# Kernel optimization log

Measured on AMD Instinct MI355X. Metric: run time of the kernel, lower is better.

Reference implementation:

```python
import jax, jax.numpy as jnp
import numpy as np

B, IN, H, OUT, E = 8192, 1024, 4096, 1024, 8
HG = H // 2  # gating hidden

def setup_inputs() -> dict:
    key = jax.random.key(0)
    ks = jax.random.split(key, 9)
    s_in = 1.0 / np.sqrt(IN)
    s_h = 1.0 / np.sqrt(H)
    s_hg = 1.0 / np.sqrt(HG)
    return {
        "x": jax.random.normal(ks[0], (B, IN), jnp.float32),
        # gating MLP: Linear(IN,HG) -> ReLU -> Linear(HG,E) -> softmax
        "gw1": jax.random.uniform(ks[1], (IN, HG), jnp.float32, -s_in, s_in),
        "gb1": jax.random.uniform(ks[2], (HG,), jnp.float32, -s_in, s_in),
        "gw2": jax.random.uniform(ks[3], (HG, E), jnp.float32, -s_hg, s_hg),
        "gb2": jax.random.uniform(ks[4], (E,), jnp.float32, -s_hg, s_hg),
        # experts: E x (Linear(IN,H) -> ReLU -> Linear(H,OUT))
        "ew1": jax.random.uniform(ks[5], (E, IN, H), jnp.float32, -s_in, s_in),
        "eb1": jax.random.uniform(ks[6], (E, H), jnp.float32, -s_in, s_in),
        "ew2": jax.random.uniform(ks[7], (E, H, OUT), jnp.float32, -s_h, s_h),
        "eb2": jax.random.uniform(ks[8], (E, OUT), jnp.float32, -s_h, s_h),
    }

def reference(x, gw1, gb1, gw2, gb2, ew1, eb1, ew2, eb2):
    # Gating network (dropout is a no-op in eval)
    gh = jax.nn.relu(x @ gw1 + gb1)                       # [B, HG]
    gates = jax.nn.softmax(gh @ gw2 + gb2, axis=1)        # [B, E]
    # All experts run on the full batch
    h = jax.nn.relu(jnp.einsum('bi,eih->beh', x, ew1) + eb1[None])  # [B, E, H]
    eo = jnp.einsum('beh,eho->beo', h, ew2) + eb2[None]             # [B, E, OUT]
    # Gate-weighted combine: (stacked * gates[...,None]).sum(dim=1)
    combined = jnp.einsum('beo,be->bo', eo, gates)        # [B, OUT]
    return combined
```

## Files before the change

### kernel.cpp

```cpp
#include <hip/hip_runtime.h>


#define DI __device__ __forceinline__

typedef _Float16 f16;
typedef _Float16 f16x8 __attribute__((ext_vector_type(8)));
typedef float f32x4 __attribute__((ext_vector_type(4)));

constexpr int BSZ  = 8192;
constexpr int IND  = 1024;
constexpr int HID  = 4096;
constexpr int OUTD = 1024;
constexpr int NE   = 8;
constexpr int HGD  = 2048;

__global__ __launch_bounds__(256) void conv_f32_f16_kernel(
    const float* __restrict__ in, f16* __restrict__ out)
{
    size_t i = ((size_t)blockIdx.x * 256 + threadIdx.x) * 8;
    const float4* p = (const float4*)(in + i);
    float4 a = p[0], b = p[1];
    f16x8 v = {(f16)a.x, (f16)a.y, (f16)a.z, (f16)a.w,
               (f16)b.x, (f16)b.y, (f16)b.z, (f16)b.w};
    *(f16x8*)(out + i) = v;
}

__global__ __launch_bounds__(256) void transpose_f32_f16_kernel(
    const float* __restrict__ W, f16* __restrict__ Wt, int K, int N)
{
    __shared__ float t[64][65];
    int n0 = blockIdx.x * 64, k0 = blockIdx.y * 64;
    int tx = threadIdx.x & 63, ty = threadIdx.x >> 6;
#pragma unroll
    for (int i = 0; i < 16; i++) {
        int k = i * 4 + ty;
        t[k][tx] = W[(size_t)(k0 + k) * N + n0 + tx];
    }
    __syncthreads();
#pragma unroll
    for (int i = 0; i < 16; i++) {
        int n = i * 4 + ty;
        Wt[(size_t)(n0 + n) * K + k0 + tx] = (f16)t[tx][n];
    }
}

DI void gload_lds16(const void* g, void* l)
{
    typedef const __attribute__((address_space(1))) unsigned int as1_t;
    typedef __attribute__((address_space(3))) unsigned int as3_t;
    __builtin_amdgcn_global_load_lds(
        (as1_t*)(unsigned long long)(__SIZE_TYPE__)g,
        (as3_t*)(unsigned int)(__SIZE_TYPE__)l,
        16, 0, 0);
}


#define PH(BUF, MH, KS, PRE, STAGE, VM)                                        \
  {                                                                            \
    f16x8 av0 = ldA(BUF, 0, MH, KS);                                           \
    f16x8 av1 = ldA(BUF, 1, MH, KS);                                           \
    f16x8 av2 = ldA(BUF, 2, MH, KS);                                           \
    f16x8 av3 = ldA(BUF, 3, MH, KS);                                           \
    if constexpr ((PRE) >= 0) {                                                \
      _Pragma("unroll")                                                        \
      for (int n = 0; n < NF; n++) breg[n][KS] = ldB(BUF, n, KS);              \
    }                                                                          \
    STAGE                                                                      \
    __builtin_amdgcn_sched_barrier(0);                                         \
    __builtin_amdgcn_s_barrier();                                              \
    asm volatile("s_waitcnt lgkmcnt(0)" ::: "memory");                         \
    __builtin_amdgcn_sched_barrier(0);                                         \
    __builtin_amdgcn_s_setprio(1);                                             \
    _Pragma("unroll")                                                          \
    for (int n = 0; n < NF; n++) {                                             \
      acc[(MH)*4+0][n] = __builtin_amdgcn_mfma_f32_16x16x32_f16(av0, breg[n][KS], acc[(MH)*4+0][n], 0, 0, 0); \
      acc[(MH)*4+1][n] = __builtin_amdgcn_mfma_f32_16x16x32_f16(av1, breg[n][KS], acc[(MH)*4+1][n], 0, 0, 0); \
      acc[(MH)*4+2][n] = __builtin_amdgcn_mfma_f32_16x16x32_f16(av2, breg[n][KS], acc[(MH)*4+2][n], 0, 0, 0); \
      acc[(MH)*4+3][n] = __builtin_amdgcn_mfma_f32_16x16x32_f16(av3, breg[n][KS], acc[(MH)*4+3][n], 0, 0, 0); \
    }                                                                          \
    __builtin_amdgcn_s_setprio(0);                                             \
    VM                                                                         \
    __builtin_amdgcn_sched_barrier(0);                                         \
    __builtin_amdgcn_s_barrier();                                              \
    asm volatile("" ::: "memory");                                             \
  }

#define VMSTEP                                                                 \
  { if (i + 1 == NI) { asm volatile("s_waitcnt vmcnt(0)"); }                   \
    else if constexpr (BN == 256) { asm volatile("s_waitcnt vmcnt(4)"); }      \
    else { asm volatile("s_waitcnt vmcnt(2)"); } }

template <int BN, bool RELU, bool GATE, bool OUT_F16, bool ACCUM>
__global__ __launch_bounds__(512, 2) void gemm8p_kernel(
    const f16* __restrict__ A, const f16* __restrict__ Bt,
    const float* __restrict__ bias, const float* __restrict__ gate,
    void* __restrict__ Cptr, int M, int N, int K)
{
    constexpr int BM = 256, BK = 64;
    constexpr int NF  = BN / 64;
    constexpr int NBC = (BN * BK * 2) / 8192;
    __shared__ __align__(16) f16 sA[2][BM * BK];
    __shared__ __align__(16) f16 sB[2][BN * BK];

    const int tid = threadIdx.x, wid = tid >> 6, lane = tid & 63;
    const int wm = wid >> 2, wn = wid & 3;

    const int nwg = gridDim.x;
    const int bid = blockIdx.x;
    const int wg  = (bid & 7) * (nwg >> 3) + (bid >> 3);
    const int gx  = N / BN;
    const size_t bm = (size_t)(wg / gx) * BM;
    const size_t bn = (size_t)(wg % gx) * BN;

    f32x4 acc[8][NF] = {};
    f16x8 breg[NF][2];

    const int srow = (wid << 3) + (lane >> 3);
    const int scol = ((((lane & 7) << 4) ^ (((lane >> 3) & 7) << 4)) >> 1);
    const f16* Ab = A  + (bm + srow) * (size_t)K + scol;
    const f16* Bb = Bt + (bn + srow) * (size_t)K + scol;
    char* sAb = (char*)&sA[0][0] + wid * 1024;
    char* sBb = (char*)&sB[0][0] + wid * 1024;

    auto stA = [&](int b, int q, int t) {
        gload_lds16(Ab + (size_t)q * 64 * K + t * BK,
                    sAb + b * (BM * BK * 2) + q * 8192);
    };
    auto stB = [&](int b, int q, int t) {
        gload_lds16(Bb + (size_t)q * 64 * K + t * BK,
                    sBb + b * (BN * BK * 2) + q * 8192);
    };
    auto ldA = [&](int b, int f, int mh, int ks) -> f16x8 {
        int r  = wm * 128 + mh * 64 + f * 16 + (lane & 15);
        int kb = (((ks * 32) + ((lane >> 4) << 3)) << 1) ^ ((r & 7) << 4);
        return *(const f16x8*)((const char*)&sA[b][0] + r * 128 + kb);
    };
    auto ldB = [&](int b, int n, int ks) -> f16x8 {
        int r  = wn * (BN / 4) + n * 16 + (lane & 15);
        int kb = (((ks * 32) + ((lane >> 4) << 3)) << 1) ^ ((r & 7) << 4);
        return *(const f16x8*)((const char*)&sB[b][0] + r * 128 + kb);
    };

    const int NT = K / BK, NI = NT / 2;

#pragma unroll
    for (int q = 0; q < 4; q++) stA(0, q, 0);
#pragma unroll
    for (int q = 0; q < NBC; q++) stB(0, q, 0);
#pragma unroll
    for (int q = 0; q < NBC; q++) stB(1, q, 1);
    if constexpr (NBC == 4) { asm volatile("s_waitcnt vmcnt(4)"); }
    else                    { asm volatile("s_waitcnt vmcnt(2)"); }
    __builtin_amdgcn_s_barrier();
    asm volatile("" ::: "memory");

    for (int i = 0; i < NI; ++i) {
        const int t = 2 * i;
        const bool pf = (i + 1 < NI);
        PH(0, 0, 0, 0,
           { stA(1,0,t+1); stA(1,1,t+1); stA(1,2,t+1); stA(1,3,t+1); }, {})
        PH(0, 0, 1, 1, {}, {})
        PH(0, 1, 0, -1,
           { if (pf) { stB(0,0,t+2); stB(0,1,t+2); } }, {})
        PH(0, 1, 1, -1,
           { if (pf) { if constexpr (NBC == 4) { stB(0,2,t+2); stB(0,3,t+2); } } },
           VMSTEP)
        PH(1, 0, 0, 0,
           { if (pf) { stA(0,0,t+2); stA(0,1,t+2); stA(0,2,t+2); stA(0,3,t+2); } }, {})
        PH(1, 0, 1, 1, {}, {})
        PH(1, 1, 0, -1,
           { if (pf) { stB(1,0,t+3); stB(1,1,t+3); } }, {})
        PH(1, 1, 1, -1,
           { if (pf) { if constexpr (NBC == 4) { stB(1,2,t+3); stB(1,3,t+3); } } },
           VMSTEP)
    }

    const size_t row0 = bm + (size_t)wm * 128;
    const int col0 = (int)bn + wn * (BN / 4);
    const int c0 = lane & 15, r0 = (lane >> 4) * 4;
#pragma unroll
    for (int fm = 0; fm < 8; fm++) {
#pragma unroll
        for (int r = 0; r < 4; r++) {
            const size_t row = row0 + fm * 16 + r0 + r;
            float g = 1.0f;
            if constexpr (GATE) g = gate[row * NE];
#pragma unroll
            for (int n = 0; n < NF; n++) {
                const size_t col = (size_t)col0 + n * 16 + c0;
                float v = acc[fm][n][r] + bias[col];
                if constexpr (RELU) v = fmaxf(v, 0.0f);
                if constexpr (GATE) v *= g;
                if constexpr (OUT_F16) {
                    ((f16*)Cptr)[row * (size_t)N + col] = (f16)v;
                } else {
                    float* p = (float*)Cptr + row * (size_t)N + col;
                    *p = ACCUM ? (*p + v) : v;
                }
            }
        }
    }
}

__global__ __launch_bounds__(256) void gate_softmax_kernel(
    const f16* __restrict__ gh, const float* __restrict__ gw2,
    const float* __restrict__ gb2, float* __restrict__ gates)
{
    const int row  = blockIdx.x * 4 + (threadIdx.x >> 6);
    const int lane = threadIdx.x & 63;
    const f16* r = gh + (size_t)row * HGD;
    float acc[NE] = {};
    for (int k = lane; k < HGD; k += 64) {
        float h = (float)r[k];
        const float* w = gw2 + (size_t)k * NE;
#pragma unroll
        for (int e = 0; e < NE; e++) acc[e] = fmaf(h, w[e], acc[e]);
    }
#pragma unroll
    for (int off = 32; off > 0; off >>= 1)
#pragma unroll
        for (int e = 0; e < NE; e++) acc[e] += __shfl_down(acc[e], off, 64);
    if (lane == 0) {
        float l[NE], m = -1e30f;
#pragma unroll
        for (int e = 0; e < NE; e++) { l[e] = acc[e] + gb2[e]; m = fmaxf(m, l[e]); }
        float s = 0.f;
#pragma unroll
        for (int e = 0; e < NE; e++) { l[e] = expf(l[e] - m); s += l[e]; }
        float inv = 1.0f / s;
#pragma unroll
        for (int e = 0; e < NE; e++) gates[(size_t)row * NE + e] = l[e] * inv;
    }
}

extern "C" void kernel_launch(void* const* d_in, const int* in_sizes, int n_in,
                              void* d_out, int out_size, void* d_ws, size_t ws_size,
                              hipStream_t stream)
{
    const float* x   = (const float*)d_in[0];
    const float* gw1 = (const float*)d_in[1];
    const float* gb1 = (const float*)d_in[2];
    const float* gw2 = (const float*)d_in[3];
    const float* gb2 = (const float*)d_in[4];
    const float* ew1 = (const float*)d_in[5];
    const float* eb1 = (const float*)d_in[6];
    const float* ew2 = (const float*)d_in[7];
    const float* eb2 = (const float*)d_in[8];
    float* out = (float*)d_out;

    char* ws = (char*)d_ws;
    float* gates = (float*)ws;
    f16* x16  = (f16*)(ws + (256 << 10));
    f16* wbuf = x16 + (size_t)BSZ * IND;
    f16* hbuf = wbuf + (size_t)HID * IND;
    f16* gh   = hbuf;

    conv_f32_f16_kernel<<<(BSZ * IND) / (256 * 8), 256, 0, stream>>>(x, x16);

    transpose_f32_f16_kernel<<<dim3(HGD / 64, IND / 64), 256, 0, stream>>>(gw1, wbuf, IND, HGD);
    gemm8p_kernel<256, true, false, true, false>
        <<<(HGD / 256) * (BSZ / 256), 512, 0, stream>>>(
            x16, wbuf, gb1, nullptr, gh, BSZ, HGD, IND);

    gate_softmax_kernel<<<BSZ / 4, 256, 0, stream>>>(gh, gw2, gb2, gates);

    for (int e = 0; e < NE; e++) {
        transpose_f32_f16_kernel<<<dim3(HID / 64, IND / 64), 256, 0, stream>>>(
            ew1 + (size_t)e * IND * HID, wbuf, IND, HID);
        gemm8p_kernel<256, true, false, true, false>
            <<<(HID / 256) * (BSZ / 256), 512, 0, stream>>>(
                x16, wbuf, eb1 + (size_t)e * HID, nullptr, hbuf, BSZ, HID, IND);

        transpose_f32_f16_kernel<<<dim3(OUTD / 64, HID / 64), 256, 0, stream>>>(
            ew2 + (size_t)e * HID * OUTD, wbuf, HID, OUTD);
        if (e == 0)
            gemm8p_kernel<128, false, true, false, false>
                <<<(OUTD / 128) * (BSZ / 256), 512, 0, stream>>>(
                    hbuf, wbuf, eb2 + (size_t)e * OUTD, gates + e, out, BSZ, OUTD, HID);
        else
            gemm8p_kernel<128, false, true, false, true>
                <<<(OUTD / 128) * (BSZ / 256), 512, 0, stream>>>(
                    hbuf, wbuf, eb2 + (size_t)e * OUTD, gates + e, out, BSZ, OUTD, HID);
    }
}
```

Before: 1.429 ms.

## Restructure GEMM into 4-stage BK=32 LDS pipeline with 3-deep prefetch

Replaces the double-buffered BK=64 GEMM mainloop with a four-buffer BK=32 pipeline that keeps three K-tiles in flight via global_load_lds, using per-phase vmcnt waits. Each phase loads all 8 A fragments and NF B fragments and issues the full 8xNF MFMA block, with a new swizzled LDS layout (two rows per 128-byte line) and precomputed LDS offsets. The goal is to hide global-memory latency more deeply and simplify the fragment schedule. In exchange there are more barriers per unit of K work, higher register pressure from holding all fragments at once, and tail handling that assumes K/32 is a multiple of 4.

```diff
diff --git a/kernel.cpp b/kernel.cpp
--- a/kernel.cpp
+++ b/kernel.cpp
@@ -55,29 +55,32 @@
 }
 
 
-#define PH(BUF, MH, KS, PRE, STAGE, VM)                                        \
+#define VMAIN { if constexpr (NBC == 2) asm volatile("s_waitcnt vmcnt(8)");   \
+                else                     asm volatile("s_waitcnt vmcnt(6)"); }
+#define VMTAIL1 { if constexpr (NBC == 2) asm volatile("s_waitcnt vmcnt(4)"); \
+                  else                     asm volatile("s_waitcnt vmcnt(3)"); }
+#define VMTAIL2 { asm volatile("s_waitcnt vmcnt(0)"); }
+
+#define STG(TT, BB) { stA(BB, 0, TT); stA(BB, 1, TT); stB(BB, 0, TT);         \
+                      if constexpr (NBC == 2) stB(BB, 1, TT); }
+
+#define PHASE(B, STAGE, VM)                                                    \
   {                                                                            \
-    f16x8 av0 = ldA(BUF, 0, MH, KS);                                           \
-    f16x8 av1 = ldA(BUF, 1, MH, KS);                                           \
-    f16x8 av2 = ldA(BUF, 2, MH, KS);                                           \
-    f16x8 av3 = ldA(BUF, 3, MH, KS);                                           \
-    if constexpr ((PRE) >= 0) {                                                \
-      _Pragma("unroll")                                                        \
-      for (int n = 0; n < NF; n++) breg[n][KS] = ldB(BUF, n, KS);              \
-    }                                                                          \
+    f16x8 av[8]; f16x8 bv[NF];                                                 \
+    _Pragma("unroll") for (int f = 0; f < 8; f++)                              \
+        av[f] = *(const f16x8*)(sAc + (B) * 16384 + offA[f]);                  \
+    _Pragma("unroll") for (int n = 0; n < NF; n++)                             \
+        bv[n] = *(const f16x8*)(sBc + (B) * (BN * 64) + offB[n]);              \
     STAGE                                                                      \
     __builtin_amdgcn_sched_barrier(0);                                         \
     __builtin_amdgcn_s_barrier();                                              \
     asm volatile("s_waitcnt lgkmcnt(0)" ::: "memory");                         \
     __builtin_amdgcn_sched_barrier(0);                                         \
     __builtin_amdgcn_s_setprio(1);                                             \
-    _Pragma("unroll")                                                          \
-    for (int n = 0; n < NF; n++) {                                             \
-      acc[(MH)*4+0][n] = __builtin_amdgcn_mfma_f32_16x16x32_f16(av0, breg[n][KS], acc[(MH)*4+0][n], 0, 0, 0); \
-      acc[(MH)*4+1][n] = __builtin_amdgcn_mfma_f32_16x16x32_f16(av1, breg[n][KS], acc[(MH)*4+1][n], 0, 0, 0); \
-      acc[(MH)*4+2][n] = __builtin_amdgcn_mfma_f32_16x16x32_f16(av2, breg[n][KS], acc[(MH)*4+2][n], 0, 0, 0); \
-      acc[(MH)*4+3][n] = __builtin_amdgcn_mfma_f32_16x16x32_f16(av3, breg[n][KS], acc[(MH)*4+3][n], 0, 0, 0); \
-    }                                                                          \
+    _Pragma("unroll") for (int fm = 0; fm < 8; fm++)                           \
+      _Pragma("unroll") for (int n = 0; n < NF; n++)                           \
+        acc[fm][n] = __builtin_amdgcn_mfma_f32_16x16x32_f16(                   \
+            av[fm], bv[n], acc[fm][n], 0, 0, 0);                               \
     __builtin_amdgcn_s_setprio(0);                                             \
     VM                                                                         \
     __builtin_amdgcn_sched_barrier(0);                                         \
@@ -85,94 +88,84 @@
     asm volatile("" ::: "memory");                                             \
   }
 
-#define VMSTEP                                                                 \
-  { if (i + 1 == NI) { asm volatile("s_waitcnt vmcnt(0)"); }                   \
-    else if constexpr (BN == 256) { asm volatile("s_waitcnt vmcnt(4)"); }      \
-    else { asm volatile("s_waitcnt vmcnt(2)"); } }
-
 template <int BN, bool RELU, bool GATE, bool OUT_F16, bool ACCUM>
-__global__ __launch_bounds__(512, 2) void gemm8p_kernel(
+__global__ __launch_bounds__(512, 2) void gemm4b_kernel(
     const f16* __restrict__ A, const f16* __restrict__ Bt,
     const float* __restrict__ bias, const float* __restrict__ gate,
     void* __restrict__ Cptr, int M, int N, int K)
 {
-    constexpr int BM = 256, BK = 64;
+    constexpr int BM = 256, BK = 32;
     constexpr int NF  = BN / 64;
-    constexpr int NBC = (BN * BK * 2) / 8192;
-    __shared__ __align__(16) f16 sA[2][BM * BK];
-    __shared__ __align__(16) f16 sB[2][BN * BK];
+    constexpr int NBC = BN / 128;
+    __shared__ __align__(16) f16 sA[4][BM * BK];
+    __shared__ __align__(16) f16 sB[4][BN * BK];
+    const char* sAc = (const char*)&sA[0][0];
+    const char* sBc = (const char*)&sB[0][0];
 
     const int tid = threadIdx.x, wid = tid >> 6, lane = tid & 63;
     const int wm = wid >> 2, wn = wid & 3;
 
-    const int nwg = gridDim.x;
-    const int bid = blockIdx.x;
+    const int nwg = gridDim.x, bid = blockIdx.x;
     const int wg  = (bid & 7) * (nwg >> 3) + (bid >> 3);
     const int gx  = N / BN;
     const size_t bm = (size_t)(wg / gx) * BM;
     const size_t bn = (size_t)(wg % gx) * BN;
 
     f32x4 acc[8][NF] = {};
-    f16x8 breg[NF][2];
-
-    const int srow = (wid << 3) + (lane >> 3);
-    const int scol = ((((lane & 7) << 4) ^ (((lane >> 3) & 7) << 4)) >> 1);
-    const f16* Ab = A  + (bm + srow) * (size_t)K + scol;
-    const f16* Bb = Bt + (bn + srow) * (size_t)K + scol;
-    char* sAb = (char*)&sA[0][0] + wid * 1024;
-    char* sBb = (char*)&sB[0][0] + wid * 1024;
-
-    auto stA = [&](int b, int q, int t) {
-        gload_lds16(Ab + (size_t)q * 64 * K + t * BK,
-                    sAb + b * (BM * BK * 2) + q * 8192);
+
+    const int sP   = tid >> 3;
+    const int offp = (((tid >> 2) & 1) << 6) | ((tid & 3) << 4);
+    const int offl = offp ^ ((sP & 7) << 4);
+    const int srow = (sP << 1) | (offl >> 6);
+    const int skel = (offl & 63) >> 1;
+    const f16* pA = A  + (bm + srow) * (size_t)K + skel;
+    const f16* pB = Bt + (bn + srow) * (size_t)K + skel;
+
+    auto stA = [&](int b, int q, int T) {
+        gload_lds16(pA + (size_t)(q * 128) * K + (size_t)T * BK,
+                    (char*)sAc + b * 16384 + q * 8192 + wid * 1024);
     };
-    auto stB = [&](int b, int q, int t) {
-        gload_lds16(Bb + (size_t)q * 64 * K + t * BK,
-                    sBb + b * (BN * BK * 2) + q * 8192);
+    auto stB = [&](int b, int q, int T) {
+        gload_lds16(pB + (size_t)(q * 128) * K + (size_t)T * BK,
+                    (char*)sBc + b * (BN * 64) + q * 8192 + wid * 1024);
     };
-    auto ldA = [&](int b, int f, int mh, int ks) -> f16x8 {
-        int r  = wm * 128 + mh * 64 + f * 16 + (lane & 15);
-        int kb = (((ks * 32) + ((lane >> 4) << 3)) << 1) ^ ((r & 7) << 4);
-        return *(const f16x8*)((const char*)&sA[b][0] + r * 128 + kb);
-    };
-    auto ldB = [&](int b, int n, int ks) -> f16x8 {
-        int r  = wn * (BN / 4) + n * 16 + (lane & 15);
-        int kb = (((ks * 32) + ((lane >> 4) << 3)) << 1) ^ ((r & 7) << 4);
-        return *(const f16x8*)((const char*)&sB[b][0] + r * 128 + kb);
-    };
-
-    const int NT = K / BK, NI = NT / 2;
-
-#pragma unroll
-    for (int q = 0; q < 4; q++) stA(0, q, 0);
-#pragma unroll
-    for (int q = 0; q < NBC; q++) stB(0, q, 0);
-#pragma unroll
-    for (int q = 0; q < NBC; q++) stB(1, q, 1);
-    if constexpr (NBC == 4) { asm volatile("s_waitcnt vmcnt(4)"); }
-    else                    { asm volatile("s_waitcnt vmcnt(2)"); }
+
+    int offA[8], offB[NF];
+    const int ks4 = (lane >> 4) << 4;
+#pragma unroll
+    for (int f = 0; f < 8; f++) {
+        int r = wm * 128 + f * 16 + (lane & 15);
+        int s = r >> 1;
+        offA[f] = s * 128 + ((((r & 1) << 6) | ks4) ^ ((s & 7) << 4));
+    }
+#pragma unroll
+    for (int n = 0; n < NF; n++) {
+        int r = wn * (BN / 4) + n * 16 + (lane & 15);
+        int s = r >> 1;
+        offB[n] = s * 128 + ((((r & 1) << 6) | ks4) ^ ((s & 7) << 4));
+    }
+
+    const int NT = K / BK, NI = NT / 4;
+
+    STG(0, 0) STG(1, 1) STG(2, 2)
+    if constexpr (NBC == 2) { asm volatile("s_waitcnt vmcnt(8)"); }
+    else                    { asm volatile("s_waitcnt vmcnt(6)"); }
     __builtin_amdgcn_s_barrier();
     asm volatile("" ::: "memory");
 
-    for (int i = 0; i < NI; ++i) {
-        const int t = 2 * i;
-        const bool pf = (i + 1 < NI);
-        PH(0, 0, 0, 0,
-           { stA(1,0,t+1); stA(1,1,t+1); stA(1,2,t+1); stA(1,3,t+1); }, {})
-        PH(0, 0, 1, 1, {}, {})
-        PH(0, 1, 0, -1,
-           { if (pf) { stB(0,0,t+2); stB(0,1,t+2); } }, {})
-        PH(0, 1, 1, -1,
-           { if (pf) { if constexpr (NBC == 4) { stB(0,2,t+2); stB(0,3,t+2); } } },
-           VMSTEP)
-        PH(1, 0, 0, 0,
-           { if (pf) { stA(0,0,t+2); stA(0,1,t+2); stA(0,2,t+2); stA(0,3,t+2); } }, {})
-        PH(1, 0, 1, 1, {}, {})
-        PH(1, 1, 0, -1,
-           { if (pf) { stB(1,0,t+3); stB(1,1,t+3); } }, {})
-        PH(1, 1, 1, -1,
-           { if (pf) { if constexpr (NBC == 4) { stB(1,2,t+3); stB(1,3,t+3); } } },
-           VMSTEP)
+    for (int i = 0; i < NI - 1; ++i) {
+        const int T = 4 * i;
+        PHASE(0, STG(T + 3, 3), VMAIN)
+        PHASE(1, STG(T + 4, 0), VMAIN)
+        PHASE(2, STG(T + 5, 1), VMAIN)
+        PHASE(3, STG(T + 6, 2), VMAIN)
+    }
+    {
+        const int T = NT - 4;
+        PHASE(0, STG(T + 3, 3), VMAIN)
+        PHASE(1, {}, VMTAIL1)
+        PHASE(2, {}, VMTAIL2)
+        PHASE(3, {}, {})
     }
 
     const size_t row0 = bm + (size_t)wm * 128;
@@ -258,7 +251,7 @@
     conv_f32_f16_kernel<<<(BSZ * IND) / (256 * 8), 256, 0, stream>>>(x, x16);
 
     transpose_f32_f16_kernel<<<dim3(HGD / 64, IND / 64), 256, 0, stream>>>(gw1, wbuf, IND, HGD);
-    gemm8p_kernel<256, true, false, true, false>
+    gemm4b_kernel<256, true, false, true, false>
         <<<(HGD / 256) * (BSZ / 256), 512, 0, stream>>>(
             x16, wbuf, gb1, nullptr, gh, BSZ, HGD, IND);
 
@@ -267,18 +260,18 @@
     for (int e = 0; e < NE; e++) {
         transpose_f32_f16_kernel<<<dim3(HID / 64, IND / 64), 256, 0, stream>>>(
             ew1 + (size_t)e * IND * HID, wbuf, IND, HID);
-        gemm8p_kernel<256, true, false, true, false>
+        gemm4b_kernel<256, true, false, true, false>
             <<<(HID / 256) * (BSZ / 256), 512, 0, stream>>>(
                 x16, wbuf, eb1 + (size_t)e * HID, nullptr, hbuf, BSZ, HID, IND);
 
         transpose_f32_f16_kernel<<<dim3(OUTD / 64, HID / 64), 256, 0, stream>>>(
             ew2 + (size_t)e * HID * OUTD, wbuf, HID, OUTD);
         if (e == 0)
-            gemm8p_kernel<128, false, true, false, false>
+            gemm4b_kernel<128, false, true, false, false>
                 <<<(OUTD / 128) * (BSZ / 256), 512, 0, stream>>>(
                     hbuf, wbuf, eb2 + (size_t)e * OUTD, gates + e, out, BSZ, OUTD, HID);
         else
-            gemm8p_kernel<128, false, true, false, true>
+            gemm4b_kernel<128, false, true, false, true>
                 <<<(OUTD / 128) * (BSZ / 256), 512, 0, stream>>>(
                     hbuf, wbuf, eb2 + (size_t)e * OUTD, gates + e, out, BSZ, OUTD, HID);
     }
```

New measurement: 1.433 ms. Within noise of the previous version (+0.3%).
